# Kernel tuning notes

Hardware: AMD Instinct MI355X
Metric: run time of the kernel (lower is better)

The kernel has to match this reference:

```python
import jax, jax.numpy as jnp
import numpy as np
from functools import partial

STRIDES = (8, 16, 32)
SIZES = ((80, 80), (40, 40), (20, 20))
NUM_CLASSES = 80
NMS_THR = 0.65
SCORE_THR = 0.01
MAX_DET = 100  # fixed-size NMS output (padded; validity = scores > 0)


def setup_inputs() -> dict:
    key = jax.random.key(0)
    ks = jax.random.split(key, 9)
    B = 32
    out = {}
    for i, (h, w) in enumerate(SIZES):
        out[f"cls{i}"] = jax.random.normal(ks[3 * i], (B, NUM_CLASSES, h, w), jnp.float32)
        out[f"reg{i}"] = jax.random.normal(ks[3 * i + 1], (B, 4, h, w), jnp.float32)
        out[f"obj{i}"] = jax.random.normal(ks[3 * i + 2], (B, 1, h, w), jnp.float32)
    return out


def _grid_points():
    # MlvlPointGenerator.grid_priors(with_stride=True), offset=0: (x, y, stride, stride)
    pts = []
    for (h, w), s in zip(SIZES, STRIDES):
        xs = jnp.arange(w, dtype=jnp.float32) * s
        ys = jnp.arange(h, dtype=jnp.float32) * s
        xx, yy = jnp.meshgrid(xs, ys)  # [h, w], x varies fastest -> matches NHWC flatten
        st = jnp.full((h * w,), float(s), jnp.float32)
        pts.append(jnp.stack([xx.ravel(), yy.ravel(), st, st], axis=-1))
    return jnp.concatenate(pts, axis=0)  # [A, 4]


def _flatten(t, c):
    # [N, C, H, W] -> [N, H*W, C]  (permute(0,2,3,1).reshape)
    return t.transpose(0, 2, 3, 1).reshape(t.shape[0], -1, c)


def _decode(points, reg):
    # YOLOXBBoxDecoder: center = pred_xy * stride + point, wh = exp(pred_wh) * stride
    stride = points[:, 2:]                       # [A, 2]
    xys = reg[..., :2] * stride + points[:, :2]  # [B, A, 2]
    whs = jnp.exp(reg[..., 2:]) * stride         # [B, A, 2]
    return jnp.concatenate([xys - whs * 0.5, xys + whs * 0.5], axis=-1)  # x1y1x2y2


def _iou_one_vs_all(b, boxes):
    # b: [4], boxes: [A, 4]
    tl = jnp.maximum(b[:2], boxes[:, :2])
    br = jnp.minimum(b[2:], boxes[:, 2:])
    wh = jnp.clip(br - tl, 0.0)
    inter = wh[:, 0] * wh[:, 1]
    a1 = (b[2] - b[0]) * (b[3] - b[1])
    a2 = (boxes[:, 2] - boxes[:, 0]) * (boxes[:, 3] - boxes[:, 1])
    return inter / (a1 + a2 - inter + 1e-6)


def _nms_image(boxes, cls_scores, objectness):
    # boxes [A,4], cls_scores [A,C] (post-sigmoid), objectness [A] (post-sigmoid)
    max_scores = jnp.max(cls_scores, axis=1)
    labels = jnp.argmax(cls_scores, axis=1)
    scores = max_scores * objectness
    live = jnp.where(scores >= SCORE_THR, scores, -jnp.inf)  # score_thr filter

    # batched_nms: offset boxes per class so boxes of different labels never overlap
    offset = jax.lax.stop_gradient(jnp.max(jnp.abs(boxes)) + 1.0)
    boxes_off = jax.lax.stop_gradient(boxes) + labels.astype(boxes.dtype)[:, None] * offset

    def body(i, state):
        live, keep, kscores = state
        best = jnp.argmax(live)
        kscores = kscores.at[i].set(live[best])
        keep = keep.at[i].set(best)
        iou = _iou_one_vs_all(boxes_off[best], boxes_off)
        live = jnp.where(iou > NMS_THR, -jnp.inf, live)
        live = live.at[best].set(-jnp.inf)
        return live, keep, kscores

    keep0 = jnp.zeros((MAX_DET,), jnp.int32)
    ks0 = jnp.full((MAX_DET,), -jnp.inf, boxes.dtype)
    _, keep, kscores = jax.lax.fori_loop(0, MAX_DET, body, (live, keep0, ks0))

    valid = kscores > -jnp.inf
    out_boxes = jnp.where(valid[:, None], boxes[keep], 0.0)
    out_scores = jnp.where(valid, scores[keep], 0.0)
    out_labels = jnp.where(valid, labels[keep], -1)
    return out_boxes, out_scores, out_labels, valid


def _forward(cls0, cls1, cls2, reg0, reg1, reg2, obj0, obj1, obj2):
    B = cls0.shape[0]
    flat_cls = jax.nn.sigmoid(jnp.concatenate([_flatten(c, NUM_CLASSES) for c in (cls0, cls1, cls2)], axis=1))
    flat_reg = jnp.concatenate([_flatten(r, 4) for r in (reg0, reg1, reg2)], axis=1)
    flat_obj = jax.nn.sigmoid(jnp.concatenate([_flatten(o, 1) for o in (obj0, obj1, obj2)], axis=1))[..., 0]
    points = _grid_points()
    boxes = _decode(points, flat_reg)  # [B, A, 4]
    return jax.vmap(_nms_image)(boxes, flat_cls, flat_obj)


@jax.jit
def reference(cls0, cls1, cls2, reg0, reg1, reg2, obj0, obj1, obj2):
    return _forward(cls0, cls1, cls2, reg0, reg1, reg2, obj0, obj1, obj2)
```

## Files before the change

### kernel.cpp

```cpp
#include <hip/hip_runtime.h>
#include <cmath>

typedef unsigned int uint;
typedef unsigned long long ull;

#define BATCH 32
#define NA 8400
#define NC 80
#define MAXDET 100
#define NMSTHR 0.65f
#define SCTHR 0.01f
#define NEG_INF (-INFINITY)

#define NT 1024
#define NW (NT / 64)
#define EPT 9
#define NBINS 4096
#define CAP 512

__device__ __forceinline__ float stable_sigmoid(float x) {
    if (x >= 0.f) return 1.f / (1.f + expf(-x));
    float e = expf(x);
    return e / (1.f + e);
}

template<int HW, int W, int S>
__device__ __forceinline__ void decode4(
    const float* __restrict__ cls, const float* __restrict__ reg,
    const float* __restrict__ obj, int b, int p, int q, int ag,
    float4* __restrict__ wboxes, int* __restrict__ wlabels, uint* __restrict__ wkeys)
{
    const float* cbase = cls + (size_t)b * NC * HW + (size_t)(q * 20) * HW + p;
    float v[20];
    #pragma unroll
    for (int i = 0; i < 20; ++i) v[i] = cbase[(size_t)i * HW];
    float m = v[0]; int c = 0;
    #pragma unroll
    for (int i = 1; i < 20; ++i)
        if (v[i] > m) { m = v[i]; c = i; }
    c += q * 20;

    #pragma unroll
    for (int o = 1; o <= 2; o <<= 1) {
        float om = __shfl_xor(m, o);
        int   oc = __shfl_xor(c, o);
        if (om > m || (om == m && oc < c)) { m = om; c = oc; }
    }

    if (q == 0) {
        const float* rb = reg + (size_t)b * 4 * HW + p;
        float r0 = rb[0];
        float r1 = rb[HW];
        float r2 = rb[2 * (size_t)HW];
        float r3 = rb[3 * (size_t)HW];
        float ov = obj[(size_t)b * HW + p];

        int y = p / W;
        int x = p - y * W;
        float sc = stable_sigmoid(m) * stable_sigmoid(ov);
        float cx = r0 * (float)S + (float)x * (float)S;
        float cy = r1 * (float)S + (float)y * (float)S;
        float bw = expf(r2) * (float)S;
        float bh = expf(r3) * (float)S;

        wboxes[ag]  = make_float4(cx - bw * 0.5f, cy - bh * 0.5f,
                                  cx + bw * 0.5f, cy + bh * 0.5f);
        wlabels[ag] = c;
        wkeys[ag]   = (sc >= SCTHR) ? ~__float_as_uint(sc) : 0xFFFFFFFFu;
    }
}

__global__ __launch_bounds__(256) void decode_kernel(
    const float* __restrict__ cls0, const float* __restrict__ reg0, const float* __restrict__ obj0,
    const float* __restrict__ cls1, const float* __restrict__ reg1, const float* __restrict__ obj1,
    const float* __restrict__ cls2, const float* __restrict__ reg2, const float* __restrict__ obj2,
    float4* __restrict__ wboxes, int* __restrict__ wlabels, uint* __restrict__ wkeys)
{
    int gid = blockIdx.x * blockDim.x + threadIdx.x;
    int ag = gid >> 2;
    int q  = gid & 3;
    int b = ag / NA;
    int j = ag - b * NA;

    if (j < 6400)
        decode4<6400, 80, 8>(cls0, reg0, obj0, b, j, q, ag, wboxes, wlabels, wkeys);
    else if (j < 8000)
        decode4<1600, 40, 16>(cls1, reg1, obj1, b, j - 6400, q, ag, wboxes, wlabels, wkeys);
    else
        decode4<400, 20, 32>(cls2, reg2, obj2, b, j - 8000, q, ag, wboxes, wlabels, wkeys);
}

__global__ __launch_bounds__(NT) void nms_kernel(
    const float4* __restrict__ wboxes, const int* __restrict__ wlabels,
    const uint* __restrict__ wkeys, float* __restrict__ out)
{
    int b = blockIdx.x;
    int t = threadIdx.x;
    int lane = t & 63;
    int wv = t >> 6;
    const float4* boxes  = wboxes  + (size_t)b * NA;
    const int*    labels = wlabels + (size_t)b * NA;
    const uint*   keys   = wkeys   + (size_t)b * NA;

    __shared__ uint  s_hist[NBINS];
    __shared__ uint  s_cum[NBINS + 1];
    __shared__ uint  s_wsum[NW];
    __shared__ ull   s_skey[CAP];
    __shared__ float s_kbox[MAXDET][4];
    __shared__ float s_ka1[MAXDET];
    __shared__ int   s_kidx[MAXDET];
    __shared__ float s_kscr[MAXDET];
    __shared__ int   s_klab[MAXDET];
    __shared__ float s_red[NW];
    __shared__ float s_off;
    __shared__ int   s_kept, s_winlo, s_winhi, s_nsel;

    float m = 0.f;
    #pragma unroll
    for (int w = 0; w < EPT; ++w) {
        int e = t + w * NT;
        if (e < NA) {
            float4 v = boxes[e];
            m = fmaxf(m, fmaxf(fmaxf(fabsf(v.x), fabsf(v.y)),
                               fmaxf(fabsf(v.z), fabsf(v.w))));
        }
    }
    #pragma unroll
    for (int o = 32; o >= 1; o >>= 1) m = fmaxf(m, __shfl_xor(m, o));
    if (lane == 0) s_red[wv] = m;
    for (int i = t; i < NBINS; i += NT) s_hist[i] = 0;
    if (t == 0) { s_kept = 0; s_winlo = 0; }
    __syncthreads();
    if (t == 0) {
        float mm = 0.f;
        for (int w = 0; w < NW; ++w) mm = fmaxf(mm, s_red[w]);
        s_off = mm + 1.f;
    }
    #pragma unroll
    for (int w = 0; w < EPT; ++w) {
        int e = t + w * NT;
        if (e < NA) {
            uint k = keys[e];
            if (k != 0xFFFFFFFFu) atomicAdd(&s_hist[k >> 20], 1u);
        }
    }
    __syncthreads();
    float off = s_off;

    uint l0 = s_hist[4 * t], l1 = s_hist[4 * t + 1],
         l2 = s_hist[4 * t + 2], l3 = s_hist[4 * t + 3];
    uint L = l0 + l1 + l2 + l3;
    uint ls = L;
    #pragma unroll
    for (int o = 1; o < 64; o <<= 1) {
        uint v = __shfl_up(ls, o);
        if (lane >= o) ls += v;
    }
    if (lane == 63) s_wsum[wv] = ls;
    __syncthreads();
    if (t < NW) {
        uint v = s_wsum[t];
        uint vs = v;
        #pragma unroll
        for (int o = 1; o < NW; o <<= 1) {
            uint u = __shfl_up(vs, o);
            if ((t & 63) >= o) vs += u;
        }
        s_wsum[t] = vs - v;
    }
    __syncthreads();
    uint base = s_wsum[wv] + (ls - L);
    s_cum[4 * t]     = base;
    s_cum[4 * t + 1] = base + l0;
    s_cum[4 * t + 2] = base + l0 + l1;
    s_cum[4 * t + 3] = base + l0 + l1 + l2;
    if (t == NT - 1) s_cum[NBINS] = base + L;

    for (;;) {
        __syncthreads();
        int kept = s_kept, winlo = s_winlo;
        uint remaining = s_cum[NBINS] - s_cum[winlo];
        if (kept >= MAXDET || winlo >= NBINS || remaining == 0u) break;
        if (t == 0) { s_winhi = winlo + 1; s_nsel = 0; }
        if (t < CAP) s_skey[t] = ~0ull;
        __syncthreads();
        uint cl = s_cum[winlo];
        #pragma unroll
        for (int q = 0; q < 4; ++q) {
            int i = t + q * NT;
            if (i >= winlo && i < NBINS) {
                bool p0 = (s_cum[i + 1] - cl) <= (uint)CAP;
                bool p1 = (i + 1 < NBINS) && ((s_cum[i + 2] - cl) <= (uint)CAP);
                if (p0 && !p1) s_winhi = i + 1;
            }
        }
        __syncthreads();
        int winhi = s_winhi;

        #pragma unroll
        for (int w = 0; w < EPT; ++w) {
            int e = t + w * NT;
            bool q = false;
            uint k = 0;
            if (e < NA) {
                k = keys[e];
                if (k != 0xFFFFFFFFu) {
                    int bin = (int)(k >> 20);
                    q = (bin >= winlo && bin < winhi);
                }
            }
            ull mask = __ballot(q);
            if (mask) {
                int leader = __ffsll(mask) - 1;
                int pbase = 0;
                if (lane == leader) pbase = atomicAdd(&s_nsel, __popcll(mask));
                pbase = __shfl(pbase, leader);
                if (q) {
                    int pos = pbase + __popcll(mask & ((1ull << lane) - 1ull));
                    if (pos < CAP) s_skey[pos] = ((ull)k << 32) | (uint)e;
                }
            }
        }
        __syncthreads();
        int nsel = s_nsel; if (nsel > CAP) nsel = CAP;

        ull k = (t < CAP) ? s_skey[t] : ~0ull;
        for (int k2 = 2; k2 <= CAP; k2 <<= 1) {
            for (int j = k2 >> 1; j > 0; j >>= 1) {
                if (j >= 64) {
                    if (t < CAP) s_skey[t] = k;
                    __syncthreads();
                    if (t < CAP) {
                        ull kp = s_skey[t ^ j];
                        bool low = (t & j) == 0;
                        bool up  = (t & k2) == 0;
                        k = ((k < kp) == (low == up)) ? k : kp;
                    }
                    __syncthreads();
                } else if (t < CAP) {
                    ull kp = __shfl_xor(k, j);
                    bool low = (t & j) == 0;
                    bool up  = (t & k2) == 0;
                    k = ((k < kp) == (low == up)) ? k : kp;
                }
            }
        }
        if (t < CAP) s_skey[t] = k;
        __syncthreads();

        if (t < 64) {
            int kept2 = s_kept;
            for (int cb = 0; cb < nsel && kept2 < MAXDET; cb += 64) {
                int ci = cb + lane;
                ull sk = (ci < nsel) ? s_skey[ci] : ~0ull;
                bool has = (sk != ~0ull);
                int idx = 0, lab = 0;
                float sc = 0.f, c0 = 0.f, c1 = 0.f, c2 = 0.f, c3 = 0.f, ca = 0.f;
                if (has) {
                    idx = (int)(sk & 0xFFFFFFFFull);
                    sc  = __uint_as_float(~(uint)(sk >> 32));
                    float4 rb = boxes[idx];
                    lab = labels[idx];
                    float lo = (float)lab * off;
                    c0 = rb.x + lo; c1 = rb.y + lo; c2 = rb.z + lo; c3 = rb.w + lo;
                    ca = (c2 - c0) * (c3 - c1);
                    for (int q = 0; q < kept2; ++q) {
                        float tlx = fmaxf(s_kbox[q][0], c0);
                        float tly = fmaxf(s_kbox[q][1], c1);
                        float brx = fminf(s_kbox[q][2], c2);
                        float bry = fminf(s_kbox[q][3], c3);
                        float ww = fmaxf(brx - tlx, 0.f);
                        float hh = fmaxf(bry - tly, 0.f);
                        float inter = ww * hh;
                        float iou = inter / (s_ka1[q] + ca - inter + 1e-6f);
                        if (iou > NMSTHR) { has = false; break; }
                    }
                }
                ull am = __ballot(has);
                while (am && kept2 < MAXDET) {
                    int f = __ffsll(am) - 1;
                    float f0 = __shfl(c0, f), f1 = __shfl(c1, f);
                    float f2 = __shfl(c2, f), f3 = __shfl(c3, f);
                    float fa = __shfl(ca, f);
                    int   fidx = __shfl(idx, f);
                    int   flab = __shfl(lab, f);
                    float fsc  = __shfl(sc, f);
                    if (lane == 0) {
                        s_kbox[kept2][0] = f0; s_kbox[kept2][1] = f1;
                        s_kbox[kept2][2] = f2; s_kbox[kept2][3] = f3;
                        s_ka1[kept2] = fa; s_kidx[kept2] = fidx;
                        s_kscr[kept2] = fsc; s_klab[kept2] = flab;
                    }
                    kept2++;
                    if (lane == f) has = false;
                    if (has) {
                        float tlx = fmaxf(f0, c0), tly = fmaxf(f1, c1);
                        float brx = fminf(f2, c2), bry = fminf(f3, c3);
                        float ww = fmaxf(brx - tlx, 0.f), hh = fmaxf(bry - tly, 0.f);
                        float inter = ww * hh;
                        float iou = inter / (fa + ca - inter + 1e-6f);
                        if (iou > NMSTHR) has = false;
                    }
                    am = __ballot(has);
                }
            }
            if (lane == 0) s_kept = kept2;
        }
        __syncthreads();
        if (t == 0) s_winlo = s_winhi;
    }
    __syncthreads();

    if (t < MAXDET) {
        int kept = s_kept;
        float4 obx = make_float4(0.f, 0.f, 0.f, 0.f);
        float osc = 0.f, olab = -1.f, oval = 0.f;
        if (t < kept) {
            int idx = s_kidx[t];
            obx  = boxes[idx];
            osc  = s_kscr[t];
            olab = (float)s_klab[t];
            oval = 1.f;
        }
        float* ob = out + ((size_t)b * MAXDET + t) * 4;
        ob[0] = obx.x; ob[1] = obx.y; ob[2] = obx.z; ob[3] = obx.w;
        out[BATCH * MAXDET * 4 + b * MAXDET + t] = osc;
        out[BATCH * MAXDET * 5 + b * MAXDET + t] = olab;
        out[BATCH * MAXDET * 6 + b * MAXDET + t] = oval;
    }
}

extern "C" void kernel_launch(void* const* d_in, const int* in_sizes, int n_in,
                              void* d_out, int out_size, void* d_ws, size_t ws_size,
                              hipStream_t stream) {
    const float* cls0 = (const float*)d_in[0];
    const float* reg0 = (const float*)d_in[1];
    const float* obj0 = (const float*)d_in[2];
    const float* cls1 = (const float*)d_in[3];
    const float* reg1 = (const float*)d_in[4];
    const float* obj1 = (const float*)d_in[5];
    const float* cls2 = (const float*)d_in[6];
    const float* reg2 = (const float*)d_in[7];
    const float* obj2 = (const float*)d_in[8];

    char* ws = (char*)d_ws;
    size_t nBA = (size_t)BATCH * NA;
    float4* wboxes  = (float4*)ws;
    int*    wlabels = (int*)(ws + nBA * 16);
    uint*   wkeys   = (uint*)(ws + nBA * 20);

    int total = BATCH * NA * 4;
    decode_kernel<<<total / 256, 256, 0, stream>>>(
        cls0, reg0, obj0, cls1, reg1, obj1, cls2, reg2, obj2,
        wboxes, wlabels, wkeys);

    nms_kernel<<<BATCH, NT, 0, stream>>>(wboxes, wlabels, wkeys, (float*)d_out);
}
```

Before: 172.0 us.

## Refine histogram binning of score keys and precompute intra-chunk IoU suppression masks

Histogram bins move from the top 12 bits of the score key to a finer mapping over the high-score float range, so the candidate window selected per round should hold fewer, tighter elements and need fewer rounds. Inside each 64-candidate chunk, every lane now precomputes a 64-bit IoU suppression mask against all other lanes up front. The serial greedy loop then only tests mask bits instead of doing shuffles and an IoU each step. The cost is 64 full IoU evaluations per lane even when few candidates survive.

```diff
diff --git a/kernel.cpp b/kernel.cpp
--- a/kernel.cpp
+++ b/kernel.cpp
@@ -22,6 +22,13 @@
     if (x >= 0.f) return 1.f / (1.f + expf(-x));
     float e = expf(x);
     return e / (1.f + e);
+}
+
+__device__ __forceinline__ int key2bin(uint k) {
+    uint sb = ~k;
+    uint s = (sb >= 0x3C000000u) ? ((sb - 0x3C000000u) >> 14) : 0u;
+    if (s > 4095u) s = 4095u;
+    return (int)(4095u - s);
 }
 
 template<int HW, int W, int S>
@@ -141,7 +148,7 @@
         int e = t + w * NT;
         if (e < NA) {
             uint k = keys[e];
-            if (k != 0xFFFFFFFFu) atomicAdd(&s_hist[k >> 20], 1u);
+            if (k != 0xFFFFFFFFu) atomicAdd(&s_hist[key2bin(k)], 1u);
         }
     }
     __syncthreads();
@@ -205,7 +212,7 @@
             if (e < NA) {
                 k = keys[e];
                 if (k != 0xFFFFFFFFu) {
-                    int bin = (int)(k >> 20);
+                    int bin = key2bin(k);
                     q = (bin >= winlo && bin < winhi);
                 }
             }
@@ -253,10 +260,10 @@
             for (int cb = 0; cb < nsel && kept2 < MAXDET; cb += 64) {
                 int ci = cb + lane;
                 ull sk = (ci < nsel) ? s_skey[ci] : ~0ull;
-                bool has = (sk != ~0ull);
+                bool alive = (sk != ~0ull);
                 int idx = 0, lab = 0;
                 float sc = 0.f, c0 = 0.f, c1 = 0.f, c2 = 0.f, c3 = 0.f, ca = 0.f;
-                if (has) {
+                if (alive) {
                     idx = (int)(sk & 0xFFFFFFFFull);
                     sc  = __uint_as_float(~(uint)(sk >> 32));
                     float4 rb = boxes[idx];
@@ -273,35 +280,35 @@
                         float hh = fmaxf(bry - tly, 0.f);
                         float inter = ww * hh;
                         float iou = inter / (s_ka1[q] + ca - inter + 1e-6f);
-                        if (iou > NMSTHR) { has = false; break; }
+                        if (iou > NMSTHR) { alive = false; break; }
                     }
                 }
-                ull am = __ballot(has);
+                ull my_supp = 0;
+                for (int j = 0; j < 64; ++j) {
+                    float p0 = __shfl(c0, j), p1 = __shfl(c1, j);
+                    float p2 = __shfl(c2, j), p3 = __shfl(c3, j);
+                    float pa = __shfl(ca, j);
+                    float tlx = fmaxf(p0, c0), tly = fmaxf(p1, c1);
+                    float brx = fminf(p2, c2), bry = fminf(p3, c3);
+                    float ww = fmaxf(brx - tlx, 0.f), hh = fmaxf(bry - tly, 0.f);
+                    float inter = ww * hh;
+                    float iou = inter / (pa + ca - inter + 1e-6f);
+                    if (iou > NMSTHR) my_supp |= (1ull << j);
+                }
+                ull am = __ballot(alive);
                 while (am && kept2 < MAXDET) {
                     int f = __ffsll(am) - 1;
-                    float f0 = __shfl(c0, f), f1 = __shfl(c1, f);
-                    float f2 = __shfl(c2, f), f3 = __shfl(c3, f);
-                    float fa = __shfl(ca, f);
-                    int   fidx = __shfl(idx, f);
-                    int   flab = __shfl(lab, f);
-                    float fsc  = __shfl(sc, f);
-                    if (lane == 0) {
-                        s_kbox[kept2][0] = f0; s_kbox[kept2][1] = f1;
-                        s_kbox[kept2][2] = f2; s_kbox[kept2][3] = f3;
-                        s_ka1[kept2] = fa; s_kidx[kept2] = fidx;
-                        s_kscr[kept2] = fsc; s_klab[kept2] = flab;
+                    if (lane == f) {
+                        s_kbox[kept2][0] = c0; s_kbox[kept2][1] = c1;
+                        s_kbox[kept2][2] = c2; s_kbox[kept2][3] = c3;
+                        s_ka1[kept2] = ca; s_kidx[kept2] = idx;
+                        s_kscr[kept2] = sc; s_klab[kept2] = lab;
+                        alive = false;
+                    } else if (alive && ((my_supp >> f) & 1ull)) {
+                        alive = false;
                     }
                     kept2++;
-                    if (lane == f) has = false;
-                    if (has) {
-                        float tlx = fmaxf(f0, c0), tly = fmaxf(f1, c1);
-                        float brx = fminf(f2, c2), bry = fminf(f3, c3);
-                        float ww = fmaxf(brx - tlx, 0.f), hh = fmaxf(bry - tly, 0.f);
-                        float inter = ww * hh;
-                        float iou = inter / (fa + ca - inter + 1e-6f);
-                        if (iou > NMSTHR) has = false;
-                    }
-                    am = __ballot(has);
+                    am = __ballot(alive);
                 }
             }
             if (lane == 0) s_kept = kept2;
```

New measurement: 174.9 us. About the same (+1.7%).
